# Performance work log

Measured on AMD Instinct MI355X. Metric: run time of the kernel, lower is better.

The kernel has to match this reference:

```python
import jax, jax.numpy as jnp
import numpy as np

HEADS = 4
OUT_DIM = 64
NEG_SLOPE = 0.2


def setup_inputs() -> dict:
    key = jax.random.key(0)
    k1, k2, k3, k4 = jax.random.split(key, 4)
    n, in_dim = 4096, 256
    x = jax.random.normal(k1, (n, in_dim), dtype=jnp.float32)
    adj = jax.random.randint(k2, (n, n), 0, 2, dtype=jnp.int32)
    # lin: in_dim -> heads*out_dim (no bias), stored as [in_dim, heads*out_dim]
    W = jax.random.normal(k3, (in_dim, HEADS * OUT_DIM), dtype=jnp.float32) * 0.05
    # att_weight: [heads, 2*out_dim]
    att = jax.random.normal(k4, (HEADS, 2 * OUT_DIM), dtype=jnp.float32) * 0.05
    return {"x": x, "adj": adj, "W": W, "att": att}


def reference(x, adj, W, att):
    n = x.shape[0]
    h = (x @ W).reshape(n, HEADS, OUT_DIM)  # [n, H, D]
    # scores[i,j,h] = att[h] . cat(h_i, h_j) = <h_i, a_src[h]> + <h_j, a_dst[h]>
    a_src, a_dst = att[:, :OUT_DIM], att[:, OUT_DIM:]
    e_src = jnp.einsum('nhd,hd->nh', h, a_src)  # [n, H]
    e_dst = jnp.einsum('nhd,hd->nh', h, a_dst)  # [n, H]
    scores = e_src[:, None, :] + e_dst[None, :, :]  # [n, n, H]
    scores = jax.nn.leaky_relu(scores, negative_slope=NEG_SLOPE)
    mask = (adj > 0)[:, :, None]  # [n, n, 1]
    scores = jnp.where(mask, scores, -jnp.inf)
    alpha = jax.nn.softmax(scores, axis=1)  # softmax over neighbors j
    # h_prime[i,h,d] = sum_j alpha[i,j,h] * h[j,h,d]
    h_prime = jnp.einsum('ijh,jhd->ihd', alpha, h)
    return h_prime.reshape(n, HEADS * OUT_DIM)
```

## Files before the change

kernel.cpp:

```cpp
#include <hip/hip_runtime.h>
#include <hip/hip_bf16.h>

#define HEADS 4
#define ODIM 64
#define HD 256
#define NEG_SLOPE 0.2f
#define SPLITS 4
#define BJ 128

typedef __attribute__((ext_vector_type(8))) short bf16x8;
typedef __attribute__((ext_vector_type(4))) float floatx4;
typedef __attribute__((ext_vector_type(2))) float floatx2;

__global__ __launch_bounds__(256) void pack_xw(const float* __restrict__ x,
                                               const float* __restrict__ W,
                                               const int* __restrict__ adj,
                                               __hip_bfloat16* __restrict__ xh,
                                               __hip_bfloat16* __restrict__ xl,
                                               __hip_bfloat16* __restrict__ wh,
                                               __hip_bfloat16* __restrict__ wl,
                                               unsigned long long* __restrict__ adjP,
                                               int K, int n, int nxb, int nwb) {
    const int b = blockIdx.x;
    const int Kc = K >> 5;
    if (b < nxb) {
        const int g = b * 256 + threadIdx.x;
        const int lane = g & 63, frag = g >> 6;
        const int kc = frag % Kc, mc = frag / Kc;
        const int l16 = lane & 15, q = lane >> 4;
        const float* src = x + (size_t)(mc * 16 + l16) * K + kc * 32 + q * 8;
        const float4 v0 = *(const float4*)src;
        const float4 v1 = *(const float4*)(src + 4);
        const float vv[8] = {v0.x, v0.y, v0.z, v0.w, v1.x, v1.y, v1.z, v1.w};
        union { __hip_bfloat16 b[8]; bf16x8 v; } H, L;
        #pragma unroll
        for (int p = 0; p < 8; ++p) {
            H.b[p] = __float2bfloat16(vv[p]);
            L.b[p] = __float2bfloat16(vv[p] - __bfloat162float(H.b[p]));
        }
        *(bf16x8*)&xh[(size_t)frag * 512 + lane * 8] = H.v;
        *(bf16x8*)&xl[(size_t)frag * 512 + lane * 8] = L.v;
    } else if (b < nxb + nwb) {
        const int g = (b - nxb) * 256 + threadIdx.x;
        const int lane = g & 63, frag = g >> 6;
        const int kc = frag % Kc, nc = frag / Kc;
        const int l16 = lane & 15, q = lane >> 4;
        union { __hip_bfloat16 b[8]; bf16x8 v; } H, L;
        #pragma unroll
        for (int p = 0; p < 8; ++p) {
            const float w = W[(size_t)(kc * 32 + q * 8 + p) * HD + nc * 16 + l16];
            H.b[p] = __float2bfloat16(w);
            L.b[p] = __float2bfloat16(w - __bfloat162float(H.b[p]));
        }
        *(bf16x8*)&wh[(size_t)frag * 512 + lane * 8] = H.v;
        *(bf16x8*)&wl[(size_t)frag * 512 + lane * 8] = L.v;
    } else {
        const int row = b - nxb - nwb;
        const int wv = threadIdx.x >> 6, ln = threadIdx.x & 63;
        const int* ar = adj + (size_t)row * n;
        unsigned long long* dst = adjP + (size_t)row * (n >> 6);
        #pragma unroll 4
        for (int s = 0; s < 16; ++s) {
            const int seg = wv * 16 + s;
            const int v = ar[seg * 64 + ln];
            const unsigned long long m = __ballot(v > 0);
            if (ln == 0) dst[seg] = m;
        }
    }
}

__global__ __launch_bounds__(128) void gemm_fused(
    const __hip_bfloat16* __restrict__ xh, const __hip_bfloat16* __restrict__ xl,
    const __hip_bfloat16* __restrict__ wh, const __hip_bfloat16* __restrict__ wl,
    const float* __restrict__ att, float4* __restrict__ E4,
    __hip_bfloat16* __restrict__ hbB, int n, int K) {

    __shared__ __hip_bfloat16 T[64][40];

    const int tid = threadIdx.x, wave = tid >> 6, lane = tid & 63;
    const int q = lane >> 4, l16 = lane & 15;
    const int m0 = blockIdx.x * 32;
    const int head = blockIdx.y;
    const int Kc = K >> 5;
    const int mc = (m0 >> 4) + wave;

    floatx4 acc[4] = {{0.f,0.f,0.f,0.f},{0.f,0.f,0.f,0.f},{0.f,0.f,0.f,0.f},{0.f,0.f,0.f,0.f}};

    const __hip_bfloat16* Axh = xh + (size_t)mc * Kc * 512 + lane * 8;
    const __hip_bfloat16* Axl = xl + (size_t)mc * Kc * 512 + lane * 8;
    const __hip_bfloat16* Bwh = wh + lane * 8;
    const __hip_bfloat16* Bwl = wl + lane * 8;
    #pragma unroll 2
    for (int kc = 0; kc < Kc; ++kc) {
        const bf16x8 ah = *(const bf16x8*)(Axh + (size_t)kc * 512);
        const bf16x8 al = *(const bf16x8*)(Axl + (size_t)kc * 512);
        bf16x8 bh[4], bl[4];
        #pragma unroll
        for (int nt = 0; nt < 4; ++nt) {
            const size_t fo = (size_t)((head * 4 + nt) * Kc + kc) * 512;
            bh[nt] = *(const bf16x8*)(Bwh + fo);
            bl[nt] = *(const bf16x8*)(Bwl + fo);
        }
        #pragma unroll
        for (int nt = 0; nt < 4; ++nt)
            acc[nt] = __builtin_amdgcn_mfma_f32_16x16x32_bf16(ah, bh[nt], acc[nt], 0, 0, 0);
        #pragma unroll
        for (int nt = 0; nt < 4; ++nt)
            acc[nt] = __builtin_amdgcn_mfma_f32_16x16x32_bf16(ah, bl[nt], acc[nt], 0, 0, 0);
        #pragma unroll
        for (int nt = 0; nt < 4; ++nt)
            acc[nt] = __builtin_amdgcn_mfma_f32_16x16x32_bf16(al, bh[nt], acc[nt], 0, 0, 0);
    }

    float as_v[4], ad_v[4];
    #pragma unroll
    for (int nt = 0; nt < 4; ++nt) {
        as_v[nt] = att[head * 2 * ODIM + nt * 16 + l16];
        ad_v[nt] = att[head * 2 * ODIM + ODIM + nt * 16 + l16];
    }
    #pragma unroll
    for (int r = 0; r < 4; ++r) {
        float ps = 0.f, pd = 0.f;
        #pragma unroll
        for (int nt = 0; nt < 4; ++nt) {
            ps = fmaf(acc[nt][r], as_v[nt], ps);
            pd = fmaf(acc[nt][r], ad_v[nt], pd);
        }
        #pragma unroll
        for (int m = 1; m <= 8; m <<= 1) {
            ps += __shfl_xor(ps, m, 64);
            pd += __shfl_xor(pd, m, 64);
        }
        if (l16 == 0) {
            const int i = m0 + wave * 16 + q * 4 + r;
            E4[i * HEADS + head] = make_float4(__expf(ps), __expf(NEG_SLOPE * ps),
                                               __expf(pd), __expf(NEG_SLOPE * pd));
        }
    }

    #pragma unroll
    for (int nt = 0; nt < 4; ++nt) {
        union { __hip_bfloat16 b[4]; uint2 u; } pk;
        #pragma unroll
        for (int r = 0; r < 4; ++r) pk.b[r] = __float2bfloat16(acc[nt][r]);
        *(uint2*)&T[nt * 16 + l16][wave * 16 + q * 4] = pk.u;
    }
    __syncthreads();

    #pragma unroll
    for (int ffi = 0; ffi < 2; ++ffi) {
        const int f = wave + ffi * 2;
        const bf16x8 v = *(const bf16x8*)&T[f * 16 + l16][q * 8];
        const size_t frag = ((size_t)head * (n >> 5) + (m0 >> 5)) * 4 + f;
        *(bf16x8*)&hbB[frag * 512 + lane * 8] = v;
    }
}

__global__ __launch_bounds__(256, 2) void aggregate(
    const unsigned int* __restrict__ adjP32, const float4* __restrict__ E4,
    const __hip_bfloat16* __restrict__ hbB, float* __restrict__ outsp,
    float* __restrict__ densp, int n, int KR) {

    __shared__ unsigned short adjL[2][32][136];
    __shared__ float2 EdL[2][HEADS][BJ];

    const int tid = threadIdx.x;
    const int wave = tid >> 6, lane = tid & 63;
    const int q = lane >> 4, l16 = lane & 15, q8 = (lane >> 4) * 8;
    const int i0 = blockIdx.x * 32;
    const int K0 = blockIdx.y * KR;

    const int r8 = tid >> 3, seg = tid & 7;
    const int je = tid >> 1, heb = (tid & 1) * 2;

    floatx2 es12[2];
    #pragma unroll
    for (int mt = 0; mt < 2; ++mt) {
        const float4 e = E4[(i0 + mt * 16 + l16) * HEADS + wave];
        es12[mt][0] = e.x; es12[mt][1] = e.y;
    }

    union { short s[8]; bf16x8 v; } bones;
    #pragma unroll
    for (int p = 0; p < 8; ++p) bones.s[p] = (l16 == 0) ? (short)0x3F80 : (short)0;

    floatx4 acc[2][4];
    floatx4 accd[2];
    #pragma unroll
    for (int mt = 0; mt < 2; ++mt) {
        accd[mt] = (floatx4){0.f, 0.f, 0.f, 0.f};
        #pragma unroll
        for (int nt = 0; nt < 4; ++nt) acc[mt][nt] = (floatx4){0.f, 0.f, 0.f, 0.f};
    }

    const unsigned int* aP = adjP32 + (size_t)(i0 + r8) * (n >> 5);
    const size_t fragbase = (size_t)wave * (n >> 5) * 4;

    unsigned int awA, awB;
    float4 evA0, evA1, evB0, evB1;

    auto loadPref = [&](int jc, unsigned int& aw, float4& e0, float4& e1) {
        aw = aP[(jc >> 5) + (seg >> 1)];
        e0 = E4[(jc + je) * HEADS + heb];
        e1 = E4[(jc + je) * HEADS + heb + 1];
    };
    auto stage = [&](int buf, unsigned int aw, const float4& e0, const float4& e1) {
        const unsigned int bits = aw >> ((seg & 1) * 16);
        #pragma unroll
        for (int g2 = 0; g2 < 2; ++g2) {
            uint4 u;
            u.x = ((bits >> (g2*8+0)) & 1u ? 0xFFFFu : 0u) | ((bits >> (g2*8+1)) & 1u ? 0xFFFF0000u : 0u);
            u.y = ((bits >> (g2*8+2)) & 1u ? 0xFFFFu : 0u) | ((bits >> (g2*8+3)) & 1u ? 0xFFFF0000u : 0u);
            u.z = ((bits >> (g2*8+4)) & 1u ? 0xFFFFu : 0u) | ((bits >> (g2*8+5)) & 1u ? 0xFFFF0000u : 0u);
            u.w = ((bits >> (g2*8+6)) & 1u ? 0xFFFFu : 0u) | ((bits >> (g2*8+7)) & 1u ? 0xFFFF0000u : 0u);
            *(uint4*)&adjL[buf][r8][seg * 16 + g2 * 8] = u;
        }
        EdL[buf][heb][je]     = make_float2(e0.z, e0.w);
        EdL[buf][heb + 1][je] = make_float2(e1.z, e1.w);
    };

    auto computeChunk = [&](int buf, int jc) {
        bf16x8 bA[4], bB[4];
        #pragma unroll
        for (int nt = 0; nt < 4; ++nt)
            bA[nt] = *(const bf16x8*)&hbB[(fragbase + (size_t)(jc >> 5) * 4 + nt) * 512 + lane * 8];
        #pragma unroll
        for (int ks = 0; ks < 4; ++ks) {
            const bf16x8* bcur = (ks & 1) ? bB : bA;
            bf16x8* bnxt = (ks & 1) ? bA : bB;
            if (ks < 3) {
                #pragma unroll
                for (int nt = 0; nt < 4; ++nt)
                    bnxt[nt] = *(const bf16x8*)&hbB[(fragbase + (size_t)((jc >> 5) + ks + 1) * 4 + nt) * 512 + lane * 8];
            }
            const float4* ep = (const float4*)&EdL[buf][wave][ks * 32 + q8];
            const float4 e01 = ep[0], e23 = ep[1], e45 = ep[2], e67 = ep[3];
            floatx2 ed[8];
            ed[0][0]=e01.x; ed[0][1]=e01.y;  ed[1][0]=e01.z; ed[1][1]=e01.w;
            ed[2][0]=e23.x; ed[2][1]=e23.y;  ed[3][0]=e23.z; ed[3][1]=e23.w;
            ed[4][0]=e45.x; ed[4][1]=e45.y;  ed[5][0]=e45.z; ed[5][1]=e45.w;
            ed[6][0]=e67.x; ed[6][1]=e67.y;  ed[7][0]=e67.z; ed[7][1]=e67.w;
            #pragma unroll
            for (int mt = 0; mt < 2; ++mt) {
                const uint4 msk = *(const uint4*)&adjL[buf][mt * 16 + l16][ks * 32 + q8];
                const unsigned int mm[4] = {msk.x, msk.y, msk.z, msk.w};
                union { unsigned int u[4]; bf16x8 v; } af;
                #pragma unroll
                for (int p = 0; p < 4; ++p) {
                    const floatx2 pa = es12[mt] * ed[2 * p];
                    const floatx2 pb = es12[mt] * ed[2 * p + 1];
                    const float wa = fmaxf(pa[0], pa[1]);
                    const float wb = fmaxf(pb[0], pb[1]);
                    af.u[p] = __builtin_amdgcn_perm(__float_as_uint(wb), __float_as_uint(wa),
                                                    0x07060302u) & mm[p];
                }
                #pragma unroll
                for (int nt = 0; nt < 4; ++nt)
                    acc[mt][nt] = __builtin_amdgcn_mfma_f32_16x16x32_bf16(af.v, bcur[nt], acc[mt][nt], 0, 0, 0);
                accd[mt] = __builtin_amdgcn_mfma_f32_16x16x32_bf16(af.v, bones.v, accd[mt], 0, 0, 0);
            }
        }
    };

    const int KEND = K0 + KR;
    loadPref(K0, awA, evA0, evA1);
    loadPref(K0 + BJ < KEND ? K0 + BJ : K0, awB, evB0, evB1);
    stage(0, awA, evA0, evA1);
    __syncthreads();

    for (int jc = K0; jc < KEND; jc += 2 * BJ) {
        int j2 = jc + 2 * BJ; if (j2 >= KEND) j2 = K0;
        loadPref(j2, awA, evA0, evA1);
        computeChunk(0, jc);
        stage(1, awB, evB0, evB1);
        __syncthreads();

        int j3 = jc + 3 * BJ; if (j3 >= KEND) j3 = K0;
        loadPref(j3, awB, evB0, evB1);
        computeChunk(1, jc + BJ);
        stage(0, awA, evA0, evA1);
        __syncthreads();
    }

    const size_t sOut = (size_t)blockIdx.y * n * HD;
    #pragma unroll
    for (int mt = 0; mt < 2; ++mt)
        #pragma unroll
        for (int nt = 0; nt < 4; ++nt)
            #pragma unroll
            for (int r = 0; r < 4; ++r)
                outsp[sOut + (size_t)(i0 + mt * 16 + q * 4 + r) * HD + wave * ODIM + nt * 16 + l16] = acc[mt][nt][r];
    if (l16 == 0) {
        #pragma unroll
        for (int mt = 0; mt < 2; ++mt)
            #pragma unroll
            for (int r = 0; r < 4; ++r)
                densp[((size_t)blockIdx.y * n + i0 + mt * 16 + q * 4 + r) * HEADS + wave] = accd[mt][r];
    }
}

__global__ __launch_bounds__(256) void normalize(const float* __restrict__ outsp,
                                                 const float* __restrict__ densp,
                                                 float* __restrict__ out, int n, int splits) {
    const int g = blockIdx.x * 256 + threadIdx.x;
    const int i = g >> 6;
    const int c4 = (g & 63) * 4;
    const int head = c4 >> 6;
    float den = 0.f;
    for (int s = 0; s < splits; ++s) den += densp[((size_t)s * n + i) * HEADS + head];
    float4 v = {0.f, 0.f, 0.f, 0.f};
    for (int s = 0; s < splits; ++s) {
        const float4 t = *(const float4*)&outsp[(size_t)s * n * HD + (size_t)i * HD + c4];
        v.x += t.x; v.y += t.y; v.z += t.z; v.w += t.w;
    }
    const float inv = 1.0f / den;
    v.x *= inv; v.y *= inv; v.z *= inv; v.w *= inv;
    *(float4*)&out[(size_t)i * HD + c4] = v;
}

extern "C" void kernel_launch(void* const* d_in, const int* in_sizes, int n_in,
                              void* d_out, int out_size, void* d_ws, size_t ws_size,
                              hipStream_t stream) {
    const float* x   = (const float*)d_in[0];
    const int*   adj = (const int*)d_in[1];
    const float* W   = (const float*)d_in[2];
    const float* att = (const float*)d_in[3];
    float* out = (float*)d_out;

    const int in_dim = in_sizes[2] / HD;
    const int n = in_sizes[0] / in_dim;

    char* ws = (char*)d_ws;
    size_t off = 0;
    auto alloc = [&](size_t bytes) -> void* {
        void* p = ws + off; off += (bytes + 255) & ~(size_t)255; return p;
    };
    __hip_bfloat16* xh = (__hip_bfloat16*)alloc((size_t)n * in_dim * 2);
    __hip_bfloat16* xl = (__hip_bfloat16*)alloc((size_t)n * in_dim * 2);
    __hip_bfloat16* wh = (__hip_bfloat16*)alloc((size_t)in_dim * HD * 2);
    __hip_bfloat16* wl = (__hip_bfloat16*)alloc((size_t)in_dim * HD * 2);
    float4*         E4 = (float4*)alloc((size_t)n * HEADS * 16);
    __hip_bfloat16* hbB = (__hip_bfloat16*)alloc((size_t)n * HD * 2);
    unsigned long long* adjP = (unsigned long long*)alloc((size_t)n * (n >> 6) * 8);

    const size_t outB = (size_t)n * HD * 4, denB = (size_t)n * HEADS * 4;
    float* densp = (float*)alloc((size_t)SPLITS * denB);
    float* outsp = (float*)alloc((size_t)SPLITS * outB);

    const int nxb = (n / 16) * (in_dim / 32) * 64 / 256;
    const int nwb = (HD / 16) * (in_dim / 32) * 64 / 256;
    const int nab = n;
    pack_xw<<<nxb + nwb + nab, 256, 0, stream>>>(x, W, adj, xh, xl, wh, wl, adjP, in_dim, n, nxb, nwb);
    gemm_fused<<<dim3(n / 32, HEADS), 128, 0, stream>>>(xh, xl, wh, wl, att, E4, hbB, n, in_dim);
    aggregate<<<dim3(n / 32, SPLITS), 256, 0, stream>>>((const unsigned int*)adjP, E4, hbB, outsp, densp, n, n / SPLITS);
    normalize<<<n * 64 / 256, 256, 0, stream>>>(outsp, densp, out, n, SPLITS);
}
```

Before: 158.5 us.

## Drop LDS staging in aggregate, read adjacency bits and Ed directly per lane

New measurement: 162.2 us. 1.02x slower.

```diff
diff --git a/kernel.cpp b/kernel.cpp
--- a/kernel.cpp
+++ b/kernel.cpp
@@ -5,7 +5,6 @@
 #define ODIM 64
 #define HD 256
 #define NEG_SLOPE 0.2f
-#define SPLITS 4
 #define BJ 128
 
 typedef __attribute__((ext_vector_type(8))) short bf16x8;
@@ -72,7 +71,7 @@
 __global__ __launch_bounds__(128) void gemm_fused(
     const __hip_bfloat16* __restrict__ xh, const __hip_bfloat16* __restrict__ xl,
     const __hip_bfloat16* __restrict__ wh, const __hip_bfloat16* __restrict__ wl,
-    const float* __restrict__ att, float4* __restrict__ E4,
+    const float* __restrict__ att, float2* __restrict__ Es, float2* __restrict__ Ed,
     __hip_bfloat16* __restrict__ hbB, int n, int K) {
 
     __shared__ __hip_bfloat16 T[64][40];
@@ -133,8 +132,8 @@
         }
         if (l16 == 0) {
             const int i = m0 + wave * 16 + q * 4 + r;
-            E4[i * HEADS + head] = make_float4(__expf(ps), __expf(NEG_SLOPE * ps),
-                                               __expf(pd), __expf(NEG_SLOPE * pd));
+            Es[head * n + i] = make_float2(__expf(ps), __expf(NEG_SLOPE * ps));
+            Ed[head * n + i] = make_float2(__expf(pd), __expf(NEG_SLOPE * pd));
         }
     }
 
@@ -156,27 +155,21 @@
     }
 }
 
-__global__ __launch_bounds__(256, 2) void aggregate(
-    const unsigned int* __restrict__ adjP32, const float4* __restrict__ E4,
-    const __hip_bfloat16* __restrict__ hbB, float* __restrict__ outsp,
-    float* __restrict__ densp, int n, int KR) {
-
-    __shared__ unsigned short adjL[2][32][136];
-    __shared__ float2 EdL[2][HEADS][BJ];
+__global__ __launch_bounds__(256, 3) void aggregate(
+    const unsigned int* __restrict__ adjP32, const float2* __restrict__ Es,
+    const float2* __restrict__ Ed, const __hip_bfloat16* __restrict__ hbB,
+    float* __restrict__ outsp, float* __restrict__ densp, int n, int KR) {
 
     const int tid = threadIdx.x;
     const int wave = tid >> 6, lane = tid & 63;
-    const int q = lane >> 4, l16 = lane & 15, q8 = (lane >> 4) * 8;
+    const int q = lane >> 4, l16 = lane & 15, q8 = q * 8;
     const int i0 = blockIdx.x * 32;
     const int K0 = blockIdx.y * KR;
 
-    const int r8 = tid >> 3, seg = tid & 7;
-    const int je = tid >> 1, heb = (tid & 1) * 2;
-
     floatx2 es12[2];
     #pragma unroll
     for (int mt = 0; mt < 2; ++mt) {
-        const float4 e = E4[(i0 + mt * 16 + l16) * HEADS + wave];
+        const float2 e = Es[(size_t)wave * n + i0 + mt * 16 + l16];
         es12[mt][0] = e.x; es12[mt][1] = e.y;
     }
 
@@ -193,93 +186,64 @@
         for (int nt = 0; nt < 4; ++nt) acc[mt][nt] = (floatx4){0.f, 0.f, 0.f, 0.f};
     }
 
-    const unsigned int* aP = adjP32 + (size_t)(i0 + r8) * (n >> 5);
-    const size_t fragbase = (size_t)wave * (n >> 5) * 4;
-
-    unsigned int awA, awB;
-    float4 evA0, evA1, evB0, evB1;
-
-    auto loadPref = [&](int jc, unsigned int& aw, float4& e0, float4& e1) {
-        aw = aP[(jc >> 5) + (seg >> 1)];
-        e0 = E4[(jc + je) * HEADS + heb];
-        e1 = E4[(jc + je) * HEADS + heb + 1];
+    const unsigned int* aR0 = adjP32 + (size_t)(i0 + l16) * (n >> 5);
+    const unsigned int* aR1 = adjP32 + (size_t)(i0 + 16 + l16) * (n >> 5);
+    const float2* edp = Ed + (size_t)wave * n;
+    const __hip_bfloat16* hb = hbB + ((size_t)wave * (n >> 5) * 4) * 512 + lane * 8;
+
+    const int ksBase = K0 >> 5;
+    const int nks = KR >> 5;
+    const int NG = nks >> 2;
+
+    float4 edb[2][4];
+    bf16x8 hbb[2][4];
+    auto ldks = [&](int s, int b) {
+        const float4* ev = (const float4*)(edp + (size_t)s * 32 + q8);
+        #pragma unroll
+        for (int p = 0; p < 4; ++p) edb[b][p] = ev[p];
+        #pragma unroll
+        for (int nt = 0; nt < 4; ++nt)
+            hbb[b][nt] = *(const bf16x8*)(hb + (size_t)(s * 4 + nt) * 512);
     };
-    auto stage = [&](int buf, unsigned int aw, const float4& e0, const float4& e1) {
-        const unsigned int bits = aw >> ((seg & 1) * 16);
-        #pragma unroll
-        for (int g2 = 0; g2 < 2; ++g2) {
-            uint4 u;
-            u.x = ((bits >> (g2*8+0)) & 1u ? 0xFFFFu : 0u) | ((bits >> (g2*8+1)) & 1u ? 0xFFFF0000u : 0u);
-            u.y = ((bits >> (g2*8+2)) & 1u ? 0xFFFFu : 0u) | ((bits >> (g2*8+3)) & 1u ? 0xFFFF0000u : 0u);
-            u.z = ((bits >> (g2*8+4)) & 1u ? 0xFFFFu : 0u) | ((bits >> (g2*8+5)) & 1u ? 0xFFFF0000u : 0u);
-            u.w = ((bits >> (g2*8+6)) & 1u ? 0xFFFFu : 0u) | ((bits >> (g2*8+7)) & 1u ? 0xFFFF0000u : 0u);
-            *(uint4*)&adjL[buf][r8][seg * 16 + g2 * 8] = u;
-        }
-        EdL[buf][heb][je]     = make_float2(e0.z, e0.w);
-        EdL[buf][heb + 1][je] = make_float2(e1.z, e1.w);
-    };
-
-    auto computeChunk = [&](int buf, int jc) {
-        bf16x8 bA[4], bB[4];
-        #pragma unroll
-        for (int nt = 0; nt < 4; ++nt)
-            bA[nt] = *(const bf16x8*)&hbB[(fragbase + (size_t)(jc >> 5) * 4 + nt) * 512 + lane * 8];
-        #pragma unroll
-        for (int ks = 0; ks < 4; ++ks) {
-            const bf16x8* bcur = (ks & 1) ? bB : bA;
-            bf16x8* bnxt = (ks & 1) ? bA : bB;
-            if (ks < 3) {
-                #pragma unroll
-                for (int nt = 0; nt < 4; ++nt)
-                    bnxt[nt] = *(const bf16x8*)&hbB[(fragbase + (size_t)((jc >> 5) + ks + 1) * 4 + nt) * 512 + lane * 8];
-            }
-            const float4* ep = (const float4*)&EdL[buf][wave][ks * 32 + q8];
-            const float4 e01 = ep[0], e23 = ep[1], e45 = ep[2], e67 = ep[3];
-            floatx2 ed[8];
-            ed[0][0]=e01.x; ed[0][1]=e01.y;  ed[1][0]=e01.z; ed[1][1]=e01.w;
-            ed[2][0]=e23.x; ed[2][1]=e23.y;  ed[3][0]=e23.z; ed[3][1]=e23.w;
-            ed[4][0]=e45.x; ed[4][1]=e45.y;  ed[5][0]=e45.z; ed[5][1]=e45.w;
-            ed[6][0]=e67.x; ed[6][1]=e67.y;  ed[7][0]=e67.z; ed[7][1]=e67.w;
+
+    ldks(ksBase, 0);
+    uint4 a0c = *(const uint4*)&aR0[ksBase];
+    uint4 a1c = *(const uint4*)&aR1[ksBase];
+
+    for (int g = 0; g < NG; ++g) {
+        const int gn = (g + 1 < NG) ? g + 1 : 0;
+        const uint4 a0n = *(const uint4*)&aR0[ksBase + gn * 4];
+        const uint4 a1n = *(const uint4*)&aR1[ksBase + gn * 4];
+        #pragma unroll
+        for (int k4 = 0; k4 < 4; ++k4) {
+            const int s = ksBase + g * 4 + k4;
+            const int sn = (g * 4 + k4 + 1 < nks) ? s + 1 : ksBase;
+            ldks(sn, (k4 + 1) & 1);
+            const int cb = k4 & 1;
+            const unsigned int w0 = k4 == 0 ? a0c.x : k4 == 1 ? a0c.y : k4 == 2 ? a0c.z : a0c.w;
+            const unsigned int w1 = k4 == 0 ? a1c.x : k4 == 1 ? a1c.y : k4 == 2 ? a1c.z : a1c.w;
             #pragma unroll
             for (int mt = 0; mt < 2; ++mt) {
-                const uint4 msk = *(const uint4*)&adjL[buf][mt * 16 + l16][ks * 32 + q8];
-                const unsigned int mm[4] = {msk.x, msk.y, msk.z, msk.w};
+                const unsigned int wmt = mt ? w1 : w0;
                 union { unsigned int u[4]; bf16x8 v; } af;
                 #pragma unroll
                 for (int p = 0; p < 4; ++p) {
-                    const floatx2 pa = es12[mt] * ed[2 * p];
-                    const floatx2 pb = es12[mt] * ed[2 * p + 1];
-                    const float wa = fmaxf(pa[0], pa[1]);
-                    const float wb = fmaxf(pb[0], pb[1]);
+                    const float4 e = edb[cb][p];
+                    const float wa = fmaxf(es12[mt][0] * e.x, es12[mt][1] * e.y);
+                    const float wb = fmaxf(es12[mt][0] * e.z, es12[mt][1] * e.w);
+                    const unsigned int sh = wmt >> (q8 + 2 * p);
+                    const unsigned int mm = ((sh & 1u) ? 0xFFFFu : 0u) |
+                                            ((sh & 2u) ? 0xFFFF0000u : 0u);
                     af.u[p] = __builtin_amdgcn_perm(__float_as_uint(wb), __float_as_uint(wa),
-                                                    0x07060302u) & mm[p];
+                                                    0x07060302u) & mm;
                 }
                 #pragma unroll
                 for (int nt = 0; nt < 4; ++nt)
-                    acc[mt][nt] = __builtin_amdgcn_mfma_f32_16x16x32_bf16(af.v, bcur[nt], acc[mt][nt], 0, 0, 0);
+                    acc[mt][nt] = __builtin_amdgcn_mfma_f32_16x16x32_bf16(af.v, hbb[cb][nt], acc[mt][nt], 0, 0, 0);
                 accd[mt] = __builtin_amdgcn_mfma_f32_16x16x32_bf16(af.v, bones.v, accd[mt], 0, 0, 0);
             }
         }
-    };
-
-    const int KEND = K0 + KR;
-    loadPref(K0, awA, evA0, evA1);
-    loadPref(K0 + BJ < KEND ? K0 + BJ : K0, awB, evB0, evB1);
-    stage(0, awA, evA0, evA1);
-    __syncthreads();
-
-    for (int jc = K0; jc < KEND; jc += 2 * BJ) {
-        int j2 = jc + 2 * BJ; if (j2 >= KEND) j2 = K0;
-        loadPref(j2, awA, evA0, evA1);
-        computeChunk(0, jc);
-        stage(1, awB, evB0, evB1);
-        __syncthreads();
-
-        int j3 = jc + 3 * BJ; if (j3 >= KEND) j3 = K0;
-        loadPref(j3, awB, evB0, evB1);
-        computeChunk(1, jc + BJ);
-        stage(0, awA, evA0, evA1);
-        __syncthreads();
+        a0c = a0n; a1c = a1n;
     }
 
     const size_t sOut = (size_t)blockIdx.y * n * HD;
@@ -339,19 +303,23 @@
     __hip_bfloat16* xl = (__hip_bfloat16*)alloc((size_t)n * in_dim * 2);
     __hip_bfloat16* wh = (__hip_bfloat16*)alloc((size_t)in_dim * HD * 2);
     __hip_bfloat16* wl = (__hip_bfloat16*)alloc((size_t)in_dim * HD * 2);
-    float4*         E4 = (float4*)alloc((size_t)n * HEADS * 16);
+    float2*         Es = (float2*)alloc((size_t)HEADS * n * 8);
+    float2*         Ed = (float2*)alloc((size_t)HEADS * n * 8);
     __hip_bfloat16* hbB = (__hip_bfloat16*)alloc((size_t)n * HD * 2);
     unsigned long long* adjP = (unsigned long long*)alloc((size_t)n * (n >> 6) * 8);
 
     const size_t outB = (size_t)n * HD * 4, denB = (size_t)n * HEADS * 4;
-    float* densp = (float*)alloc((size_t)SPLITS * denB);
-    float* outsp = (float*)alloc((size_t)SPLITS * outB);
+    int splits = 8;
+    if (ws_size && off + (size_t)splits * ((outB + 255 & ~(size_t)255) + (denB + 255 & ~(size_t)255)) > ws_size)
+        splits = 4;
+    float* densp = (float*)alloc((size_t)splits * denB);
+    float* outsp = (float*)alloc((size_t)splits * outB);
 
     const int nxb = (n / 16) * (in_dim / 32) * 64 / 256;
     const int nwb = (HD / 16) * (in_dim / 32) * 64 / 256;
     const int nab = n;
     pack_xw<<<nxb + nwb + nab, 256, 0, stream>>>(x, W, adj, xh, xl, wh, wl, adjP, in_dim, n, nxb, nwb);
-    gemm_fused<<<dim3(n / 32, HEADS), 128, 0, stream>>>(xh, xl, wh, wl, att, E4, hbB, n, in_dim);
-    aggregate<<<dim3(n / 32, SPLITS), 256, 0, stream>>>((const unsigned int*)adjP, E4, hbB, outsp, densp, n, n / SPLITS);
-    normalize<<<n * 64 / 256, 256, 0, stream>>>(outsp, densp, out, n, SPLITS);
-}
+    gemm_fused<<<dim3(n / 32, HEADS), 128, 0, stream>>>(xh, xl, wh, wl, att, Es, Ed, hbB, n, in_dim);
+    aggregate<<<dim3(n / 32, splits), 256, 0, stream>>>((const unsigned int*)adjP, Es, Ed, hbB, outsp, densp, n, n / splits);
+    normalize<<<n * 64 / 256, 256, 0, stream>>>(outsp, densp, out, n, splits);
+}
```
